# Kernel optimization log

Hardware: AMD Instinct MI355X
Metric: run time of the kernel (lower is better)

The kernel has to match this reference:

```python
import jax, jax.numpy as jnp
import numpy as np

NUM_HEADS = 8
NEG_INF = -1e9

def setup_inputs() -> dict:
    key = jax.random.key(0)
    k1, k2 = jax.random.split(key)
    B, S, D = 2, 4096, 512
    inputs = jax.random.normal(k1, (B, S, D), dtype=jnp.float32)
    # glorot-style scale for the fused QKV weight
    qkv_weights = jax.random.normal(k2, (D, 3 * D), dtype=jnp.float32) * (1.0 / np.sqrt(D))
    return {"inputs": inputs, "qkv_weights": qkv_weights}

def reference(inputs, qkv_weights):
    B, S, D = inputs.shape
    H = NUM_HEADS
    d = D // H  # head dim
    qkv = jnp.einsum('bsd,de->bse', inputs, qkv_weights)  # (B,S,3D)
    q, k, v = jnp.split(qkv, 3, axis=-1)
    # (B,S,D) -> (B,H,S,d)
    def split_heads(x):
        return x.reshape(B, S, H, d).transpose(0, 2, 1, 3)
    q, k, v = split_heads(q), split_heads(k), split_heads(v)
    scores = jnp.einsum('bhid,bhjd->bhij', q, k) / jnp.sqrt(jnp.asarray(d, inputs.dtype))
    # causal mask as in source: tril * scores + (-1e9) * upper-triangle
    tril = jnp.tril(jnp.ones((S, S), dtype=inputs.dtype))
    scores = tril * scores + NEG_INF * (1.0 - tril)
    a = jax.nn.softmax(scores, axis=-1)
    out = jnp.einsum('bhij,bhjd->bhid', a, v)  # (B,H,S,d)
    return out.transpose(0, 2, 1, 3).reshape(B, S, D)
```

## Files before the change

kernel.cpp:

```cpp
#include <hip/hip_runtime.h>

typedef unsigned short u16;
typedef __bf16 b16;
typedef b16 b16x8 __attribute__((ext_vector_type(8)));
typedef float f32x4 __attribute__((ext_vector_type(4)));
typedef u16 u16x4 __attribute__((ext_vector_type(4)));
typedef u16 u16x8 __attribute__((ext_vector_type(8)));
typedef float f4 __attribute__((ext_vector_type(4)));

#define NH 8
#define SEQ 4096
#define DM 512
#define HDIM 64
#define GM 8192
#define GK 512
#define GN 1536

#define QSCALE 0.18033688011112042f
#define SMBIAS 14.0f

__device__ __forceinline__ u16 f2bf(float f) {
  b16 h = (b16)f;
  return __builtin_bit_cast(u16, h);
}

__device__ __forceinline__ void gl16(const u16* g, u16* l) {
  __builtin_amdgcn_global_load_lds((const __attribute__((address_space(1))) void*)g,
                                   (__attribute__((address_space(3))) void*)l, 16, 0, 0);
}

__global__ __launch_bounds__(256) void cvt_fused(const float* __restrict__ x,
                                                 u16* __restrict__ y,
                                                 const float* __restrict__ w,
                                                 u16* __restrict__ wt) {
  __shared__ float tile[32][33];
  int bid = blockIdx.x;
  int t = threadIdx.x;
  if (bid < 2048) {
    int i = (bid * 256 + t) * 8;
    f4 a = *(const f4*)(x + i);
    f4 b = *(const f4*)(x + i + 4);
    u16x8 o;
    o[0] = f2bf(a[0]); o[1] = f2bf(a[1]); o[2] = f2bf(a[2]); o[3] = f2bf(a[3]);
    o[4] = f2bf(b[0]); o[5] = f2bf(b[1]); o[6] = f2bf(b[2]); o[7] = f2bf(b[3]);
    *(u16x8*)(y + i) = o;
  } else {
    int q = bid - 2048;
    int n0 = (q % 48) * 32;
    int k0 = (q / 48) * 32;
    int tn = t & 31, tk = t >> 5;
#pragma unroll
    for (int p = 0; p < 4; ++p) {
      int k = tk + p * 8;
      tile[k][tn] = w[(k0 + k) * GN + n0 + tn];
    }
    __syncthreads();
    int n_l = t >> 3, kg = (t & 7) * 4;
    u16x4 o;
#pragma unroll
    for (int i2 = 0; i2 < 4; ++i2) o[i2] = f2bf(tile[kg + i2][n_l]);
    *(u16x4*)(wt + (n0 + n_l) * GK + k0 + kg) = o;
  }
}

__global__ __launch_bounds__(256, 3) void qkv_gemm(const u16* __restrict__ A,
                                                   const u16* __restrict__ Wt,
                                                   u16* __restrict__ Q,
                                                   u16* __restrict__ K,
                                                   u16* __restrict__ Vt) {
  __shared__ __align__(16) u16 As[3][4096];
  __shared__ __align__(16) u16 Bs[3][4096];
  int bm = blockIdx.x * 128;
  int bn = blockIdx.y * 128;
  int t = threadIdx.x;
  int lane = t & 63, w = t >> 6;
  int wr = w >> 1, wc = w & 1;
  int l15 = lane & 15, g = lane >> 4;

  f32x4 acc[4][4];
#pragma unroll
  for (int i = 0; i < 4; ++i)
#pragma unroll
    for (int j = 0; j < 4; ++j) {
      acc[i][j][0] = 0.f; acc[i][j][1] = 0.f; acc[i][j][2] = 0.f; acc[i][j][3] = 0.f;
    }

#define GSTAGE(slot, k0) do {                                                   \
    _Pragma("unroll")                                                           \
    for (int p = 0; p < 2; ++p) {                                               \
      int cid = p * 256 + t;                                                    \
      int row = cid >> 2, co = (cid & 3) * 8;                                   \
      gl16(A + (size_t)(bm + row) * GK + (k0) + co, &As[slot][cid * 8]);        \
      gl16(Wt + (size_t)(bn + row) * GK + (k0) + co, &Bs[slot][cid * 8]);       \
    }                                                                           \
  } while (0)

  GSTAGE(0, 0);
  GSTAGE(1, 32);
  int cur = 0;
  for (int kk = 0; kk < 16; ++kk) {
    asm volatile("s_waitcnt vmcnt(4)" ::: "memory");
    __builtin_amdgcn_s_barrier();
    int pk = kk + 2 < 16 ? kk + 2 : 15;
    int slot = cur + 2; if (slot >= 3) slot -= 3;
    GSTAGE(slot, pk * 32);

    b16x8 af[4], bf[4];
#pragma unroll
    for (int mi = 0; mi < 4; ++mi)
      af[mi] = *(const b16x8*)(&As[cur][(wr * 64 + mi * 16 + l15) * 32 + g * 8]);
#pragma unroll
    for (int ni = 0; ni < 4; ++ni)
      bf[ni] = *(const b16x8*)(&Bs[cur][(wc * 64 + ni * 16 + l15) * 32 + g * 8]);
    __builtin_amdgcn_s_setprio(1);
#pragma unroll
    for (int mi = 0; mi < 4; ++mi)
#pragma unroll
      for (int ni = 0; ni < 4; ++ni)
        acc[mi][ni] = __builtin_amdgcn_mfma_f32_16x16x32_bf16(af[mi], bf[ni], acc[mi][ni], 0, 0, 0);
    __builtin_amdgcn_s_setprio(0);
    cur = (cur == 2) ? 0 : cur + 1;
  }

  __syncthreads();
  u16* eps = As[0];
  const int LDE = 132;
  int which = bn >> 9;
  int h0 = (bn & 511) >> 6;

  if (which < 2) {
    float scale = (which == 0) ? QSCALE : 1.0f;
#pragma unroll
    for (int mi = 0; mi < 4; ++mi)
#pragma unroll
      for (int ni = 0; ni < 4; ++ni) {
        int e_l = wc * 64 + ni * 16 + l15;
#pragma unroll
        for (int r = 0; r < 4; ++r) {
          int m = wr * 64 + mi * 16 + g * 4 + r;
          eps[m * LDE + e_l] = f2bf(acc[mi][ni][r] * scale);
        }
      }
    __syncthreads();
    u16* dst = (which == 0) ? Q : K;
#pragma unroll
    for (int pass = 0; pass < 8; ++pass) {
      int hh = pass & 1;
      int mrow = (pass >> 1) * 32 + (t >> 3);
      int chunk = t & 7;
      u16x8 v = *(const u16x8*)(eps + mrow * LDE + hh * 64 + chunk * 8);
      int mg = bm + mrow;
      int b = mg >> 12, s = mg & 4095;
      *(u16x8*)(dst + ((size_t)((b * NH + h0 + hh) * SEQ) + s) * HDIM + chunk * 8) = v;
    }
  } else {
#pragma unroll
    for (int mi = 0; mi < 4; ++mi)
#pragma unroll
      for (int ni = 0; ni < 4; ++ni) {
        int e_l = wc * 64 + ni * 16 + l15;
#pragma unroll
        for (int r = 0; r < 4; ++r) {
          int m = wr * 64 + mi * 16 + g * 4 + r;
          int pm = (m & 96) | (((m >> 2) & 3) << 3) | (((m >> 4) & 1) << 2) | (m & 3);
          eps[e_l * LDE + pm] = f2bf(acc[mi][ni][r]);
        }
      }
    __syncthreads();
#pragma unroll
    for (int pass = 0; pass < 8; ++pass) {
      int rowj = pass * 16 + (t >> 4);
      int chunk = t & 15;
      u16x8 v = *(const u16x8*)(eps + rowj * LDE + chunk * 8);
      int dd = rowj & 63, h = h0 + (rowj >> 6);
      int b = bm >> 12, s0 = bm & 4095;
      *(u16x8*)(Vt + ((size_t)((b * NH + h) * HDIM) + dd) * SEQ + s0 + chunk * 8) = v;
    }
  }
}

__global__ __launch_bounds__(256, 4) void attn(const u16* __restrict__ Q,
                                               const u16* __restrict__ Kv,
                                               const u16* __restrict__ Vtg,
                                               float* __restrict__ out) {
  int id = blockIdx.x;
  int bh = id & 15;
  int i = id >> 4;
  int j = i & 15, pp = i >> 4;
  int qt = (pp == 0) ? 63 - j : (pp == 1) ? j : (pp == 2) ? 47 - j : 16 + j;
  int b = bh >> 3, h = bh & 7;
  const u16* Qb = Q + (size_t)bh * SEQ * HDIM;
  const u16* Kb = Kv + (size_t)bh * SEQ * HDIM;
  const u16* Vb = Vtg + (size_t)bh * HDIM * SEQ;
  int t = threadIdx.x, lane = t & 63, w = t >> 6;
  int l15 = lane & 15, g = lane >> 4;
  int qb = qt * 64;
  int qw = qb + w * 16;

  __shared__ __align__(16) u16 Ks[2][4096];
  __shared__ __align__(16) u16 Vs[3][4096];

  int rsub = lane >> 3, cp = lane & 7;
  int ch = cp ^ rsub;
  int xorp = (l15 & 7) << 3;

  b16x8 qf[2];
#pragma unroll
  for (int ks = 0; ks < 2; ++ks)
    qf[ks] = *(const b16x8*)(Qb + (qw + l15) * HDIM + ks * 32 + g * 8);

  b16x8 vone;
#pragma unroll
  for (int ii = 0; ii < 8; ++ii) vone[ii] = __builtin_bit_cast(b16, (u16)0x3F80);

  f32x4 oaccT[4], lacc;
#pragma unroll
  for (int ii = 0; ii < 4; ++ii) {
    oaccT[ii][0] = 0.f; oaccT[ii][1] = 0.f; oaccT[ii][2] = 0.f; oaccT[ii][3] = 0.f;
    lacc[ii] = 0.f;
  }
  b16x8 ptp[2];

#define STAGE2(kslot, vslot, jj) do {                                           \
    _Pragma("unroll")                                                           \
    for (int p = 0; p < 2; ++p) {                                               \
      int row = (w * 2 + p) * 8 + rsub;                                         \
      gl16(Kb + (size_t)((jj) + row) * HDIM + ch * 8, &Ks[kslot][(w * 2 + p) * 512]); \
      gl16(Vb + (size_t)row * SEQ + (jj) + ch * 8, &Vs[vslot][(w * 2 + p) * 512]);   \
    }                                                                           \
  } while (0)

#define QKT(st, kslot) do {                                                     \
    _Pragma("unroll")                                                           \
    for (int c = 0; c < 4; ++c) {                                               \
      st[c][0] = -SMBIAS; st[c][1] = -SMBIAS; st[c][2] = -SMBIAS; st[c][3] = -SMBIAS; \
    }                                                                           \
    _Pragma("unroll")                                                           \
    for (int c = 0; c < 4; ++c) {                                               \
      const u16* kr = Ks[kslot] + (c * 16 + l15) * 64;                          \
      b16x8 kf0 = *(const b16x8*)(kr + ((g * 8) ^ xorp));                       \
      b16x8 kf1 = *(const b16x8*)(kr + ((32 + g * 8) ^ xorp));                  \
      st[c] = __builtin_amdgcn_mfma_f32_16x16x32_bf16(kf0, qf[0], st[c], 0, 0, 0); \
      st[c] = __builtin_amdgcn_mfma_f32_16x16x32_bf16(kf1, qf[1], st[c], 0, 0, 0); \
    }                                                                           \
  } while (0)

#define SMREG(st, jj, ptX) do {                                                 \
    if ((jj) + 63 > qw) {                                                       \
      int qq = qw + l15;                                                        \
      _Pragma("unroll")                                                         \
      for (int c = 0; c < 4; ++c)                                               \
        _Pragma("unroll")                                                       \
        for (int r = 0; r < 4; ++r) {                                           \
          int kvg = (jj) + c * 16 + g * 4 + r;                                  \
          if (kvg > qq) st[c][r] = -1e30f;                                      \
        }                                                                       \
    }                                                                           \
    _Pragma("unroll")                                                           \
    for (int c = 0; c < 4; ++c)                                                 \
      _Pragma("unroll")                                                         \
      for (int r = 0; r < 4; ++r)                                               \
        ptX[c >> 1][(c & 1) * 4 + r] = (b16)__builtin_amdgcn_exp2f(st[c][r]);   \
  } while (0)

  int nt = qt + 1;

  STAGE2(0, 0, 0);
  asm volatile("s_waitcnt vmcnt(0)" ::: "memory");
  __builtin_amdgcn_s_barrier();
  if (nt > 1) STAGE2(1, 1, 64);
  {
    f32x4 s0[4];
    QKT(s0, 0);
    SMREG(s0, 0, ptp);
  }

  for (int tt = 0; tt < nt; ++tt) {
    asm volatile("s_waitcnt vmcnt(0)" ::: "memory");
    __builtin_amdgcn_s_barrier();

    if (tt + 2 < nt) STAGE2(tt & 1, (tt + 2) % 3, (tt + 2) * 64);

    bool more = (tt + 1 < nt);
    f32x4 st[4];
    __builtin_amdgcn_s_setprio(1);
    if (more) QKT(st, (tt + 1) & 1);

    const u16* Vc = Vs[tt % 3];
#pragma unroll
    for (int ks = 0; ks < 2; ++ks) {
      int eoff = (ks * 32 + g * 8);
      lacc = __builtin_amdgcn_mfma_f32_16x16x32_bf16(vone, ptp[ks], lacc, 0, 0, 0);
#pragma unroll
      for (int tdd = 0; tdd < 4; ++tdd) {
        b16x8 vf = *(const b16x8*)(Vc + (tdd * 16 + l15) * 64 + (eoff ^ xorp));
        oaccT[tdd] = __builtin_amdgcn_mfma_f32_16x16x32_bf16(vf, ptp[ks], oaccT[tdd], 0, 0, 0);
      }
    }
    __builtin_amdgcn_s_setprio(0);

    if (more) SMREG(st, (tt + 1) * 64, ptp);
  }

  float inv = 1.0f / lacc[0];
  size_t rowbase = ((size_t)b * SEQ + qw + l15) * DM + h * HDIM;
#pragma unroll
  for (int tdd = 0; tdd < 4; ++tdd)
#pragma unroll
    for (int r = 0; r < 4; ++r)
      out[rowbase + tdd * 16 + g * 4 + r] = oaccT[tdd][r] * inv;
}

extern "C" void kernel_launch(void* const* d_in, const int* in_sizes, int n_in,
                              void* d_out, int out_size, void* d_ws, size_t ws_size,
                              hipStream_t stream) {
  const float* x = (const float*)d_in[0];
  const float* wq = (const float*)d_in[1];
  float* out = (float*)d_out;
  char* ws = (char*)d_ws;

  u16* A  = (u16*)ws;
  u16* Wt = (u16*)(ws + 8388608);
  u16* Qw = (u16*)(ws + 8388608 + 1572864);
  u16* Kw = Qw + 4194304;
  u16* Vt = Kw + 4194304;

  cvt_fused<<<2816, 256, 0, stream>>>(x, A, wq, Wt);
  dim3 gg(64, 12);
  qkv_gemm<<<gg, 256, 0, stream>>>(A, Wt, Qw, Kw, Vt);
  attn<<<1024, 256, 0, stream>>>(Qw, Kw, Vt, out);
}
```

Measured before the change: 82.77 us.

## Process two query subtiles per wave and split KV range with combine pass

The attention kernel now gives each block 128 query rows (two 64-row subtiles per wave), so each K/V tile loaded into shared memory feeds twice as many MFMAs. The KV range of each query tile is split into two segments handled by separate blocks. The first writes fp32 partial outputs straight to out, the second writes bf16 partials into a reused workspace buffer, and each records its row sums. A new normalize kernel adds the partials and divides by the combined sum, which costs an extra launch, more register pressure, and extra bf16 rounding of half the partial output.

```diff
diff --git a/kernel.cpp b/kernel.cpp
--- a/kernel.cpp
+++ b/kernel.cpp
@@ -22,6 +22,10 @@
 __device__ __forceinline__ u16 f2bf(float f) {
   b16 h = (b16)f;
   return __builtin_bit_cast(u16, h);
+}
+
+__device__ __forceinline__ float bf2f(u16 u) {
+  return __builtin_bit_cast(float, ((unsigned)u) << 16);
 }
 
 __device__ __forceinline__ void gl16(const u16* g, u16* l) {
@@ -182,20 +186,26 @@
 __global__ __launch_bounds__(256, 4) void attn(const u16* __restrict__ Q,
                                                const u16* __restrict__ Kv,
                                                const u16* __restrict__ Vtg,
-                                               float* __restrict__ out) {
+                                               float* __restrict__ out,
+                                               u16* __restrict__ Opart,
+                                               float* __restrict__ l0,
+                                               float* __restrict__ l1) {
   int id = blockIdx.x;
   int bh = id & 15;
-  int i = id >> 4;
-  int j = i & 15, pp = i >> 4;
-  int qt = (pp == 0) ? 63 - j : (pp == 1) ? j : (pp == 2) ? 47 - j : 16 + j;
+  int idx = id >> 4;
+  int seg = idx & 1;
+  int i = idx >> 1;
+  int j = i & 7, p = i >> 3;
+  int qs = (p == 0) ? 31 - j : (p == 1) ? j : (p == 2) ? 23 - j : 8 + j;
   int b = bh >> 3, h = bh & 7;
   const u16* Qb = Q + (size_t)bh * SEQ * HDIM;
   const u16* Kb = Kv + (size_t)bh * SEQ * HDIM;
   const u16* Vb = Vtg + (size_t)bh * HDIM * SEQ;
   int t = threadIdx.x, lane = t & 63, w = t >> 6;
   int l15 = lane & 15, g = lane >> 4;
-  int qb = qt * 64;
-  int qw = qb + w * 16;
+  int qb = qs * 128;
+  int ts = seg ? qs + 1 : 0;
+  int te = seg ? 2 * qs + 1 : qs;
 
   __shared__ __align__(16) u16 Ks[2][4096];
   __shared__ __align__(16) u16 Vs[3][4096];
@@ -204,50 +214,59 @@
   int ch = cp ^ rsub;
   int xorp = (l15 & 7) << 3;
 
-  b16x8 qf[2];
-#pragma unroll
-  for (int ks = 0; ks < 2; ++ks)
-    qf[ks] = *(const b16x8*)(Qb + (qw + l15) * HDIM + ks * 32 + g * 8);
+  b16x8 qf[2][2];
+#pragma unroll
+  for (int sub = 0; sub < 2; ++sub)
+#pragma unroll
+    for (int ks = 0; ks < 2; ++ks)
+      qf[sub][ks] = *(const b16x8*)(Qb + (qb + sub * 64 + w * 16 + l15) * HDIM + ks * 32 + g * 8);
 
   b16x8 vone;
 #pragma unroll
   for (int ii = 0; ii < 8; ++ii) vone[ii] = __builtin_bit_cast(b16, (u16)0x3F80);
 
-  f32x4 oaccT[4], lacc;
-#pragma unroll
-  for (int ii = 0; ii < 4; ++ii) {
-    oaccT[ii][0] = 0.f; oaccT[ii][1] = 0.f; oaccT[ii][2] = 0.f; oaccT[ii][3] = 0.f;
-    lacc[ii] = 0.f;
-  }
-  b16x8 ptp[2];
+  f32x4 oaccT[2][4], lacc[2];
+#pragma unroll
+  for (int sub = 0; sub < 2; ++sub) {
+#pragma unroll
+    for (int ii = 0; ii < 4; ++ii) {
+      oaccT[sub][ii][0] = 0.f; oaccT[sub][ii][1] = 0.f;
+      oaccT[sub][ii][2] = 0.f; oaccT[sub][ii][3] = 0.f;
+    }
+    lacc[sub][0] = 0.f; lacc[sub][1] = 0.f; lacc[sub][2] = 0.f; lacc[sub][3] = 0.f;
+  }
+  b16x8 ptp[2][2];
 
 #define STAGE2(kslot, vslot, jj) do {                                           \
     _Pragma("unroll")                                                           \
-    for (int p = 0; p < 2; ++p) {                                               \
-      int row = (w * 2 + p) * 8 + rsub;                                         \
-      gl16(Kb + (size_t)((jj) + row) * HDIM + ch * 8, &Ks[kslot][(w * 2 + p) * 512]); \
-      gl16(Vb + (size_t)row * SEQ + (jj) + ch * 8, &Vs[vslot][(w * 2 + p) * 512]);   \
+    for (int pp2 = 0; pp2 < 2; ++pp2) {                                         \
+      int row = (w * 2 + pp2) * 8 + rsub;                                       \
+      gl16(Kb + (size_t)((jj) + row) * HDIM + ch * 8, &Ks[kslot][(w * 2 + pp2) * 512]); \
+      gl16(Vb + (size_t)row * SEQ + (jj) + ch * 8, &Vs[vslot][(w * 2 + pp2) * 512]);   \
     }                                                                           \
   } while (0)
 
-#define QKT(st, kslot) do {                                                     \
+#define QKT2(sA, sB, kslot) do {                                                \
     _Pragma("unroll")                                                           \
     for (int c = 0; c < 4; ++c) {                                               \
-      st[c][0] = -SMBIAS; st[c][1] = -SMBIAS; st[c][2] = -SMBIAS; st[c][3] = -SMBIAS; \
+      sA[c][0] = -SMBIAS; sA[c][1] = -SMBIAS; sA[c][2] = -SMBIAS; sA[c][3] = -SMBIAS; \
+      sB[c][0] = -SMBIAS; sB[c][1] = -SMBIAS; sB[c][2] = -SMBIAS; sB[c][3] = -SMBIAS; \
     }                                                                           \
     _Pragma("unroll")                                                           \
     for (int c = 0; c < 4; ++c) {                                               \
       const u16* kr = Ks[kslot] + (c * 16 + l15) * 64;                          \
       b16x8 kf0 = *(const b16x8*)(kr + ((g * 8) ^ xorp));                       \
       b16x8 kf1 = *(const b16x8*)(kr + ((32 + g * 8) ^ xorp));                  \
-      st[c] = __builtin_amdgcn_mfma_f32_16x16x32_bf16(kf0, qf[0], st[c], 0, 0, 0); \
-      st[c] = __builtin_amdgcn_mfma_f32_16x16x32_bf16(kf1, qf[1], st[c], 0, 0, 0); \
+      sA[c] = __builtin_amdgcn_mfma_f32_16x16x32_bf16(kf0, qf[0][0], sA[c], 0, 0, 0); \
+      sB[c] = __builtin_amdgcn_mfma_f32_16x16x32_bf16(kf0, qf[1][0], sB[c], 0, 0, 0); \
+      sA[c] = __builtin_amdgcn_mfma_f32_16x16x32_bf16(kf1, qf[0][1], sA[c], 0, 0, 0); \
+      sB[c] = __builtin_amdgcn_mfma_f32_16x16x32_bf16(kf1, qf[1][1], sB[c], 0, 0, 0); \
     }                                                                           \
   } while (0)
 
-#define SMREG(st, jj, ptX) do {                                                 \
-    if ((jj) + 63 > qw) {                                                       \
-      int qq = qw + l15;                                                        \
+#define SMREG(st, jj, ptX, qsub) do {                                           \
+    if ((jj) + 63 > (qsub)) {                                                   \
+      int qq = (qsub) + l15;                                                    \
       _Pragma("unroll")                                                         \
       for (int c = 0; c < 4; ++c)                                               \
         _Pragma("unroll")                                                       \
@@ -263,52 +282,100 @@
         ptX[c >> 1][(c & 1) * 4 + r] = (b16)__builtin_amdgcn_exp2f(st[c][r]);   \
   } while (0)
 
-  int nt = qt + 1;
-
-  STAGE2(0, 0, 0);
+  int qsubA = qb + w * 16;
+  int qsubB = qb + 64 + w * 16;
+
+  STAGE2(ts & 1, ts % 3, ts * 64);
   asm volatile("s_waitcnt vmcnt(0)" ::: "memory");
   __builtin_amdgcn_s_barrier();
-  if (nt > 1) STAGE2(1, 1, 64);
+  if (ts < te) STAGE2((ts + 1) & 1, (ts + 1) % 3, (ts + 1) * 64);
   {
-    f32x4 s0[4];
-    QKT(s0, 0);
-    SMREG(s0, 0, ptp);
-  }
-
-  for (int tt = 0; tt < nt; ++tt) {
+    f32x4 sA[4], sB[4];
+    QKT2(sA, sB, ts & 1);
+    SMREG(sA, ts * 64, ptp[0], qsubA);
+    SMREG(sB, ts * 64, ptp[1], qsubB);
+  }
+
+  for (int tt = ts; tt <= te; ++tt) {
     asm volatile("s_waitcnt vmcnt(0)" ::: "memory");
     __builtin_amdgcn_s_barrier();
 
-    if (tt + 2 < nt) STAGE2(tt & 1, (tt + 2) % 3, (tt + 2) * 64);
-
-    bool more = (tt + 1 < nt);
-    f32x4 st[4];
+    if (tt + 2 <= te) STAGE2(tt & 1, (tt + 2) % 3, (tt + 2) * 64);
+
+    bool more = (tt < te);
+    f32x4 sA[4], sB[4];
     __builtin_amdgcn_s_setprio(1);
-    if (more) QKT(st, (tt + 1) & 1);
+    if (more) QKT2(sA, sB, (tt + 1) & 1);
 
     const u16* Vc = Vs[tt % 3];
 #pragma unroll
     for (int ks = 0; ks < 2; ++ks) {
       int eoff = (ks * 32 + g * 8);
-      lacc = __builtin_amdgcn_mfma_f32_16x16x32_bf16(vone, ptp[ks], lacc, 0, 0, 0);
+      lacc[0] = __builtin_amdgcn_mfma_f32_16x16x32_bf16(vone, ptp[0][ks], lacc[0], 0, 0, 0);
+      lacc[1] = __builtin_amdgcn_mfma_f32_16x16x32_bf16(vone, ptp[1][ks], lacc[1], 0, 0, 0);
 #pragma unroll
       for (int tdd = 0; tdd < 4; ++tdd) {
         b16x8 vf = *(const b16x8*)(Vc + (tdd * 16 + l15) * 64 + (eoff ^ xorp));
-        oaccT[tdd] = __builtin_amdgcn_mfma_f32_16x16x32_bf16(vf, ptp[ks], oaccT[tdd], 0, 0, 0);
+        oaccT[0][tdd] = __builtin_amdgcn_mfma_f32_16x16x32_bf16(vf, ptp[0][ks], oaccT[0][tdd], 0, 0, 0);
+        oaccT[1][tdd] = __builtin_amdgcn_mfma_f32_16x16x32_bf16(vf, ptp[1][ks], oaccT[1][tdd], 0, 0, 0);
       }
     }
     __builtin_amdgcn_s_setprio(0);
 
-    if (more) SMREG(st, (tt + 1) * 64, ptp);
-  }
-
-  float inv = 1.0f / lacc[0];
-  size_t rowbase = ((size_t)b * SEQ + qw + l15) * DM + h * HDIM;
-#pragma unroll
-  for (int tdd = 0; tdd < 4; ++tdd)
-#pragma unroll
-    for (int r = 0; r < 4; ++r)
-      out[rowbase + tdd * 16 + g * 4 + r] = oaccT[tdd][r] * inv;
+    if (more) {
+      SMREG(sA, (tt + 1) * 64, ptp[0], qsubA);
+      SMREG(sB, (tt + 1) * 64, ptp[1], qsubB);
+    }
+  }
+
+  if (seg == 0) {
+#pragma unroll
+    for (int sub = 0; sub < 2; ++sub) {
+      int q = qb + sub * 64 + w * 16 + l15;
+      if (g == 0) l0[bh * SEQ + q] = lacc[sub][0];
+      size_t rowbase = ((size_t)b * SEQ + q) * DM + h * HDIM;
+#pragma unroll
+      for (int tdd = 0; tdd < 4; ++tdd)
+        *(f4*)(out + rowbase + tdd * 16 + g * 4) = oaccT[sub][tdd];
+    }
+  } else {
+#pragma unroll
+    for (int sub = 0; sub < 2; ++sub) {
+      int q = qb + sub * 64 + w * 16 + l15;
+      if (g == 0) l1[bh * SEQ + q] = lacc[sub][0];
+      size_t rowbase = ((size_t)b * SEQ + q) * DM + h * HDIM;
+#pragma unroll
+      for (int tdd = 0; tdd < 4; ++tdd) {
+        u16x4 pw;
+#pragma unroll
+        for (int r = 0; r < 4; ++r) pw[r] = f2bf(oaccT[sub][tdd][r]);
+        *(u16x4*)(Opart + rowbase + tdd * 16 + g * 4) = pw;
+      }
+    }
+  }
+}
+
+__global__ __launch_bounds__(256) void normalize(float* __restrict__ out,
+                                                 const u16* __restrict__ Opart,
+                                                 const float* __restrict__ l0,
+                                                 const float* __restrict__ l1) {
+  size_t idx = ((size_t)blockIdx.x * 256 + threadIdx.x) * 8;
+  int dall = (int)(idx & 511);
+  int s = (int)((idx >> 9) & 4095);
+  int b = (int)(idx >> 21);
+  int bh = b * NH + (dall >> 6);
+  float l = l0[bh * SEQ + s] + l1[bh * SEQ + s];
+  float inv = 1.0f / l;
+  f4 v0 = *(f4*)(out + idx);
+  f4 v1 = *(f4*)(out + idx + 4);
+  u16x8 op = *(const u16x8*)(Opart + idx);
+#pragma unroll
+  for (int jj = 0; jj < 4; ++jj) {
+    v0[jj] = (v0[jj] + bf2f(op[jj])) * inv;
+    v1[jj] = (v1[jj] + bf2f(op[4 + jj])) * inv;
+  }
+  *(f4*)(out + idx) = v0;
+  *(f4*)(out + idx + 4) = v1;
 }
 
 extern "C" void kernel_launch(void* const* d_in, const int* in_sizes, int n_in,
@@ -324,9 +391,13 @@
   u16* Qw = (u16*)(ws + 8388608 + 1572864);
   u16* Kw = Qw + 4194304;
   u16* Vt = Kw + 4194304;
+  u16* Opart = A;
+  float* l0 = (float*)(ws + 8388608);
+  float* l1 = (float*)(ws + 8388608 + 262144);
 
   cvt_fused<<<2816, 256, 0, stream>>>(x, A, wq, Wt);
   dim3 gg(64, 12);
   qkv_gemm<<<gg, 256, 0, stream>>>(A, Wt, Qw, Kw, Vt);
-  attn<<<1024, 256, 0, stream>>>(Qw, Kw, Vt, out);
-}
+  attn<<<1024, 256, 0, stream>>>(Qw, Kw, Vt, out, Opart, l0, l1);
+  normalize<<<2048, 256, 0, stream>>>(out, Opart, l0, l1);
+}
```

New measurement: 126.5 us. 52.8% more time.

## Split causal attention KV range across paired blocks and combine in normalize pass

Applied to the files above, without the earlier changes.

Each attention block now handles two query tiles (p and 63-p) and processes only half of each tile's KV range, with a role bit selecting which half. This evens out per-block work under the causal mask. One half writes unnormalized fp32 output to out, the other writes bf16 partials to the workspace, and both write row sums. A new normalize kernel adds the partials and divides by the summed denominators. The cost is an extra launch and extra global traffic, and the bf16 partial adds precision loss. Combining without a running max is valid only because softmax uses a fixed bias.

```diff
diff --git a/kernel.cpp b/kernel.cpp
--- a/kernel.cpp
+++ b/kernel.cpp
@@ -22,6 +22,10 @@
 __device__ __forceinline__ u16 f2bf(float f) {
   b16 h = (b16)f;
   return __builtin_bit_cast(u16, h);
+}
+
+__device__ __forceinline__ float bf2f(u16 u) {
+  return __builtin_bit_cast(float, ((unsigned)u) << 16);
 }
 
 __device__ __forceinline__ void gl16(const u16* g, u16* l) {
@@ -182,20 +186,20 @@
 __global__ __launch_bounds__(256, 4) void attn(const u16* __restrict__ Q,
                                                const u16* __restrict__ Kv,
                                                const u16* __restrict__ Vtg,
-                                               float* __restrict__ out) {
+                                               float* __restrict__ out,
+                                               u16* __restrict__ Opart,
+                                               float* __restrict__ l0,
+                                               float* __restrict__ l1) {
   int id = blockIdx.x;
   int bh = id & 15;
-  int i = id >> 4;
-  int j = i & 15, pp = i >> 4;
-  int qt = (pp == 0) ? 63 - j : (pp == 1) ? j : (pp == 2) ? 47 - j : 16 + j;
+  int idx = id >> 4;
+  int p = idx >> 1, role = idx & 1;
   int b = bh >> 3, h = bh & 7;
   const u16* Qb = Q + (size_t)bh * SEQ * HDIM;
   const u16* Kb = Kv + (size_t)bh * SEQ * HDIM;
   const u16* Vb = Vtg + (size_t)bh * HDIM * SEQ;
   int t = threadIdx.x, lane = t & 63, w = t >> 6;
   int l15 = lane & 15, g = lane >> 4;
-  int qb = qt * 64;
-  int qw = qb + w * 16;
 
   __shared__ __align__(16) u16 Ks[2][4096];
   __shared__ __align__(16) u16 Vs[3][4096];
@@ -204,29 +208,27 @@
   int ch = cp ^ rsub;
   int xorp = (l15 & 7) << 3;
 
+  int hA = (p + 2) >> 1;
+  int hB = (64 - p) >> 1;
+  int qts[2], tss[2], tes[2];
+  qts[0] = p;      tss[0] = role ? hA : 0; tes[0] = role ? p : hA - 1;
+  qts[1] = 63 - p; tss[1] = role ? hB : 0; tes[1] = role ? 63 - p : hB - 1;
+
+  b16x8 vone;
+#pragma unroll
+  for (int ii = 0; ii < 8; ++ii) vone[ii] = __builtin_bit_cast(b16, (u16)0x3F80);
+
+  f32x4 oaccT[4], lacc;
   b16x8 qf[2];
-#pragma unroll
-  for (int ks = 0; ks < 2; ++ks)
-    qf[ks] = *(const b16x8*)(Qb + (qw + l15) * HDIM + ks * 32 + g * 8);
-
-  b16x8 vone;
-#pragma unroll
-  for (int ii = 0; ii < 8; ++ii) vone[ii] = __builtin_bit_cast(b16, (u16)0x3F80);
-
-  f32x4 oaccT[4], lacc;
-#pragma unroll
-  for (int ii = 0; ii < 4; ++ii) {
-    oaccT[ii][0] = 0.f; oaccT[ii][1] = 0.f; oaccT[ii][2] = 0.f; oaccT[ii][3] = 0.f;
-    lacc[ii] = 0.f;
-  }
   b16x8 ptp[2];
+  int qw;
 
 #define STAGE2(kslot, vslot, jj) do {                                           \
     _Pragma("unroll")                                                           \
-    for (int p = 0; p < 2; ++p) {                                               \
-      int row = (w * 2 + p) * 8 + rsub;                                         \
-      gl16(Kb + (size_t)((jj) + row) * HDIM + ch * 8, &Ks[kslot][(w * 2 + p) * 512]); \
-      gl16(Vb + (size_t)row * SEQ + (jj) + ch * 8, &Vs[vslot][(w * 2 + p) * 512]);   \
+    for (int pp2 = 0; pp2 < 2; ++pp2) {                                         \
+      int row = (w * 2 + pp2) * 8 + rsub;                                       \
+      gl16(Kb + (size_t)((jj) + row) * HDIM + ch * 8, &Ks[kslot][(w * 2 + pp2) * 512]); \
+      gl16(Vb + (size_t)row * SEQ + (jj) + ch * 8, &Vs[vslot][(w * 2 + pp2) * 512]);   \
     }                                                                           \
   } while (0)
 
@@ -263,52 +265,103 @@
         ptX[c >> 1][(c & 1) * 4 + r] = (b16)__builtin_amdgcn_exp2f(st[c][r]);   \
   } while (0)
 
-  int nt = qt + 1;
-
-  STAGE2(0, 0, 0);
-  asm volatile("s_waitcnt vmcnt(0)" ::: "memory");
-  __builtin_amdgcn_s_barrier();
-  if (nt > 1) STAGE2(1, 1, 64);
-  {
-    f32x4 s0[4];
-    QKT(s0, 0);
-    SMREG(s0, 0, ptp);
-  }
-
-  for (int tt = 0; tt < nt; ++tt) {
-    asm volatile("s_waitcnt vmcnt(0)" ::: "memory");
-    __builtin_amdgcn_s_barrier();
-
-    if (tt + 2 < nt) STAGE2(tt & 1, (tt + 2) % 3, (tt + 2) * 64);
-
-    bool more = (tt + 1 < nt);
-    f32x4 st[4];
-    __builtin_amdgcn_s_setprio(1);
-    if (more) QKT(st, (tt + 1) & 1);
-
-    const u16* Vc = Vs[tt % 3];
-#pragma unroll
-    for (int ks = 0; ks < 2; ++ks) {
-      int eoff = (ks * 32 + g * 8);
-      lacc = __builtin_amdgcn_mfma_f32_16x16x32_bf16(vone, ptp[ks], lacc, 0, 0, 0);
+#define PVT(ptX, vslot) do {                                                    \
+    const u16* Vc = Vs[vslot];                                                  \
+    _Pragma("unroll")                                                           \
+    for (int ks = 0; ks < 2; ++ks) {                                            \
+      int eoff = (ks * 32 + g * 8);                                             \
+      lacc = __builtin_amdgcn_mfma_f32_16x16x32_bf16(vone, ptX[ks], lacc, 0, 0, 0); \
+      _Pragma("unroll")                                                         \
+      for (int tdd = 0; tdd < 4; ++tdd) {                                       \
+        b16x8 vf = *(const b16x8*)(Vc + (tdd * 16 + l15) * 64 + (eoff ^ xorp)); \
+        oaccT[tdd] = __builtin_amdgcn_mfma_f32_16x16x32_bf16(vf, ptX[ks], oaccT[tdd], 0, 0, 0); \
+      }                                                                         \
+    }                                                                           \
+  } while (0)
+
+  for (int s = 0; s < 2; ++s) {
+    int qt = qts[s], ts = tss[s], te = tes[s];
+    qw = qt * 64 + w * 16;
+#pragma unroll
+    for (int ii = 0; ii < 4; ++ii) {
+      oaccT[ii][0] = 0.f; oaccT[ii][1] = 0.f; oaccT[ii][2] = 0.f; oaccT[ii][3] = 0.f;
+      lacc[ii] = 0.f;
+    }
+
+    if (s == 1) __builtin_amdgcn_s_barrier();
+
+    if (ts <= te) {
+#pragma unroll
+      for (int ks = 0; ks < 2; ++ks)
+        qf[ks] = *(const b16x8*)(Qb + (qw + l15) * HDIM + ks * 32 + g * 8);
+
+      STAGE2(ts & 1, ts % 3, ts * 64);
+      asm volatile("s_waitcnt vmcnt(0)" ::: "memory");
+      __builtin_amdgcn_s_barrier();
+      if (ts < te) STAGE2((ts + 1) & 1, (ts + 1) % 3, (ts + 1) * 64);
+      {
+        f32x4 s0[4];
+        QKT(s0, ts & 1);
+        SMREG(s0, ts * 64, ptp);
+      }
+
+      for (int tt = ts; tt <= te; ++tt) {
+        asm volatile("s_waitcnt vmcnt(0)" ::: "memory");
+        __builtin_amdgcn_s_barrier();
+
+        if (tt + 2 <= te) STAGE2(tt & 1, (tt + 2) % 3, (tt + 2) * 64);
+
+        bool more = (tt < te);
+        f32x4 st[4];
+        __builtin_amdgcn_s_setprio(1);
+        if (more) QKT(st, (tt + 1) & 1);
+        PVT(ptp, tt % 3);
+        __builtin_amdgcn_s_setprio(0);
+        if (more) SMREG(st, (tt + 1) * 64, ptp);
+      }
+    }
+
+    int q = qw + l15;
+    size_t rowbase = ((size_t)b * SEQ + q) * DM + h * HDIM;
+    if (role == 0) {
+      if (g == 0) l0[bh * SEQ + q] = lacc[0];
+#pragma unroll
+      for (int tdd = 0; tdd < 4; ++tdd)
+        *(f4*)(out + rowbase + tdd * 16 + g * 4) = oaccT[tdd];
+    } else {
+      if (g == 0) l1[bh * SEQ + q] = lacc[0];
 #pragma unroll
       for (int tdd = 0; tdd < 4; ++tdd) {
-        b16x8 vf = *(const b16x8*)(Vc + (tdd * 16 + l15) * 64 + (eoff ^ xorp));
-        oaccT[tdd] = __builtin_amdgcn_mfma_f32_16x16x32_bf16(vf, ptp[ks], oaccT[tdd], 0, 0, 0);
-      }
-    }
-    __builtin_amdgcn_s_setprio(0);
-
-    if (more) SMREG(st, (tt + 1) * 64, ptp);
-  }
-
-  float inv = 1.0f / lacc[0];
-  size_t rowbase = ((size_t)b * SEQ + qw + l15) * DM + h * HDIM;
-#pragma unroll
-  for (int tdd = 0; tdd < 4; ++tdd)
-#pragma unroll
-    for (int r = 0; r < 4; ++r)
-      out[rowbase + tdd * 16 + g * 4 + r] = oaccT[tdd][r] * inv;
+        u16x4 pw;
+#pragma unroll
+        for (int r = 0; r < 4; ++r) pw[r] = f2bf(oaccT[tdd][r]);
+        *(u16x4*)(Opart + rowbase + tdd * 16 + g * 4) = pw;
+      }
+    }
+  }
+}
+
+__global__ __launch_bounds__(256) void normalize(float* __restrict__ out,
+                                                 const u16* __restrict__ Opart,
+                                                 const float* __restrict__ l0,
+                                                 const float* __restrict__ l1) {
+  size_t idx = ((size_t)blockIdx.x * 256 + threadIdx.x) * 8;
+  int dall = (int)(idx & 511);
+  int s = (int)((idx >> 9) & 4095);
+  int b = (int)(idx >> 21);
+  int bh = b * NH + (dall >> 6);
+  float l = l0[bh * SEQ + s] + l1[bh * SEQ + s];
+  float inv = 1.0f / l;
+  f4 v0 = *(f4*)(out + idx);
+  f4 v1 = *(f4*)(out + idx + 4);
+  u16x8 op = *(const u16x8*)(Opart + idx);
+#pragma unroll
+  for (int jj = 0; jj < 4; ++jj) {
+    v0[jj] = (v0[jj] + bf2f(op[jj])) * inv;
+    v1[jj] = (v1[jj] + bf2f(op[4 + jj])) * inv;
+  }
+  *(f4*)(out + idx) = v0;
+  *(f4*)(out + idx + 4) = v1;
 }
 
 extern "C" void kernel_launch(void* const* d_in, const int* in_sizes, int n_in,
@@ -324,9 +377,13 @@
   u16* Qw = (u16*)(ws + 8388608 + 1572864);
   u16* Kw = Qw + 4194304;
   u16* Vt = Kw + 4194304;
+  u16* Opart = A;
+  float* l0 = (float*)(ws + 8388608);
+  float* l1 = (float*)(ws + 8388608 + 262144);
 
   cvt_fused<<<2816, 256, 0, stream>>>(x, A, wq, Wt);
   dim3 gg(64, 12);
   qkv_gemm<<<gg, 256, 0, stream>>>(A, Wt, Qw, Kw, Vt);
-  attn<<<1024, 256, 0, stream>>>(Qw, Kw, Vt, out);
-}
+  attn<<<1024, 256, 0, stream>>>(Qw, Kw, Vt, out, Opart, l0, l1);
+  normalize<<<2048, 256, 0, stream>>>(out, Opart, l0, l1);
+}
```

Measured after the change: 89.62 us. 8.3% more time.
